# Kernel tuning notes

Hardware: AMD Instinct MI355X
Metric: run time of the kernel (lower is better)

Reference implementation:

```python
import jax, jax.numpy as jnp
import numpy as np

D_MODEL = 2048
N_HEADS = 32
N_KV = 8
HEAD_DIM = D_MODEL // N_HEADS        # 64
N_GROUPS = N_HEADS // N_KV           # 4
ROPE_BASE = 10000.0
SCALE = HEAD_DIM ** -0.5
BATCH, SEQ = 2, 2048


def setup_inputs() -> dict:
    key = jax.random.key(0)
    k1, k2, k3, k4, k5 = jax.random.split(key, 5)
    init = 0.02  # typical transformer init scale
    return {
        "x":  jax.random.normal(k1, (BATCH, SEQ, D_MODEL), jnp.float32),
        "Wq": jax.random.normal(k2, (D_MODEL, D_MODEL), jnp.float32) * init,
        "Wk": jax.random.normal(k3, (N_KV * HEAD_DIM, D_MODEL), jnp.float32) * init,
        "Wv": jax.random.normal(k4, (N_KV * HEAD_DIM, D_MODEL), jnp.float32) * init,
        "Wo": jax.random.normal(k5, (D_MODEL, D_MODEL), jnp.float32) * init,
    }


def _apply_rope(q, k, seq_len):
    # q: (b, n_heads, s, hd), k: (b, n_kv, s, hd). LLaMA-style rotate-half RoPE.
    half = HEAD_DIM // 2
    inv_freq = 1.0 / (ROPE_BASE ** (jnp.arange(0, half, dtype=jnp.float32) / half))
    ang = jnp.arange(seq_len, dtype=jnp.float32)[:, None] * inv_freq[None, :]  # (s, half)
    cos = jnp.concatenate([jnp.cos(ang), jnp.cos(ang)], axis=-1)[None, None]   # (1,1,s,hd)
    sin = jnp.concatenate([jnp.sin(ang), jnp.sin(ang)], axis=-1)[None, None]

    def rot_half(t):
        t1, t2 = jnp.split(t, 2, axis=-1)
        return jnp.concatenate([-t2, t1], axis=-1)

    q = q * cos + rot_half(q) * sin
    k = k * cos + rot_half(k) * sin
    return q, k


def reference(x, Wq, Wk, Wv, Wo):
    b, s, _ = x.shape
    # projections (nn.Linear: y = x @ W.T)
    q = jnp.einsum('bsd,ed->bse', x, Wq).reshape(b, s, N_HEADS, HEAD_DIM).transpose(0, 2, 1, 3)
    k = jnp.einsum('bsd,ed->bse', x, Wk).reshape(b, s, N_KV, HEAD_DIM).transpose(0, 2, 1, 3)
    v = jnp.einsum('bsd,ed->bse', x, Wv).reshape(b, s, N_KV, HEAD_DIM).transpose(0, 2, 1, 3)

    q, k = _apply_rope(q, k, s)

    # GQA: repeat_interleave(k, n_groups) maps q-head h -> kv-head h // n_groups,
    # equivalent to grouping consecutive q heads and broadcasting kv per group.
    qg = q.reshape(b, N_KV, N_GROUPS, s, HEAD_DIM)
    scores = jnp.einsum('bkgqd,bkld->bkgql', qg, k) * SCALE   # (b, n_kv, g, s, s)
    attn = jax.nn.softmax(scores, axis=-1)
    out = jnp.einsum('bkgql,bkld->bkgqd', attn, v)            # (b, n_kv, g, s, hd)

    out = out.reshape(b, N_HEADS, s, HEAD_DIM).transpose(0, 2, 1, 3).reshape(b, s, D_MODEL)
    return jnp.einsum('bsd,ed->bse', out, Wo)
```

## Files before the change

kernel.cpp:

```cpp
#include <hip/hip_runtime.h>
#include <hip/hip_bf16.h>


typedef __attribute__((ext_vector_type(8))) short short8;
typedef __attribute__((ext_vector_type(4))) float f32x4;
typedef __attribute__((ext_vector_type(16))) float f32x16;

#define MFMA16(A, B, C) __builtin_amdgcn_mfma_f32_16x16x32_bf16((A), (B), (C), 0, 0, 0)
#define MFMA32(A, B, C) __builtin_amdgcn_mfma_f32_32x32x16_bf16((A), (B), (C), 0, 0, 0)

__device__ __forceinline__ ushort f2bf(float f) {
  __hip_bfloat16 h = __float2bfloat16(f);
  return __builtin_bit_cast(ushort, h);
}

__device__ __forceinline__ float fexp2(float x) {
#if __has_builtin(__builtin_amdgcn_exp2f)
  return __builtin_amdgcn_exp2f(x);
#else
  float r;
  asm("v_exp_f32 %0, %1" : "=v"(r) : "v"(x));
  return r;
#endif
}

__device__ __forceinline__ void gload_lds16(const void* g, void* l) {
  __builtin_amdgcn_global_load_lds(
      (const __attribute__((address_space(1))) unsigned int*)g,
      (__attribute__((address_space(3))) unsigned int*)l, 16, 0, 0);
}

__global__ __launch_bounds__(256) void prep_kernel(
    const float* __restrict__ x, const float* __restrict__ Wq,
    const float* __restrict__ Wk, const float* __restrict__ Wv,
    const float* __restrict__ Wo, ushort* __restrict__ xbf,
    ushort* __restrict__ wqbf, ushort* __restrict__ wkbf,
    ushort* __restrict__ wvbf, ushort* __restrict__ wobf,
    float* __restrict__ tc, float* __restrict__ ts) {
  const int blk = blockIdx.x;
  if (blk < 9216) {
    const float* src;
    ushort* dst;
    int t;
    if (blk < 4096) {
      src = x; dst = xbf; t = blk * 256 + threadIdx.x;
    } else if (blk < 6144) {
      src = Wq; dst = wqbf; t = (blk - 4096) * 256 + threadIdx.x;
    } else if (blk < 6656) {
      src = Wk; dst = wkbf; t = (blk - 6144) * 256 + threadIdx.x;
    } else if (blk < 7168) {
      src = Wv; dst = wvbf; t = (blk - 6656) * 256 + threadIdx.x;
    } else {
      src = Wo; dst = wobf; t = (blk - 7168) * 256 + threadIdx.x;
    }
    const float4* p = (const float4*)src;
    float4 a = p[t * 2], b = p[t * 2 + 1];
    int4 o;
    o.x = (int)f2bf(a.x) | ((int)f2bf(a.y) << 16);
    o.y = (int)f2bf(a.z) | ((int)f2bf(a.w) << 16);
    o.z = (int)f2bf(b.x) | ((int)f2bf(b.y) << 16);
    o.w = (int)f2bf(b.z) | ((int)f2bf(b.w) << 16);
    ((int4*)dst)[t] = o;
  } else {
    int t = (blk - 9216) * 256 + threadIdx.x;
    int j = t & 31, s = t >> 5;
    float freq = powf(10000.0f, -(float)j * (1.0f / 32.0f));
    float ang = (float)s * freq;
    tc[t] = cosf(ang);
    ts[t] = sinf(ang);
  }
}

__device__ __forceinline__ void gemm_core(const ushort* __restrict__ A,
                                          const ushort* __restrict__ Bt,
                                          int row0, int col0, int K,
                                          f32x4 (&acc)[4][4]) {
  __shared__ __align__(16) ushort As[8192];
  __shared__ __align__(16) ushort Bs[8192];
  const int t = threadIdx.x;
  const int lane = t & 63, wid = t >> 6;
  const int lr = lane & 15, lh = lane >> 4;
  const int wm = wid >> 1, wn = wid & 1;
#pragma unroll
  for (int i = 0; i < 4; ++i)
#pragma unroll
    for (int j = 0; j < 4; ++j) acc[i][j] = (f32x4){0.f, 0.f, 0.f, 0.f};

  const int srow = t >> 3, scg = (t & 7) ^ (srow & 7);
  const ushort* Asrc = A + (size_t)(row0 + srow) * K + scg * 8;
  const ushort* Bsrc = Bt + (size_t)(col0 + srow) * K + scg * 8;
  char* AsB = (char*)As + wid * 1024;
  char* BsB = (char*)Bs + wid * 1024;
  const int s7a = lr & 7;

  for (int k0 = 0; k0 < K; k0 += 64) {
    __syncthreads();
#pragma unroll
    for (int i = 0; i < 4; ++i) {
      gload_lds16(Asrc + (size_t)(32 * i) * K + k0, AsB + i * 4096);
      gload_lds16(Bsrc + (size_t)(32 * i) * K + k0, BsB + i * 4096);
    }
    __syncthreads();

    short8 af[4][2];
#pragma unroll
    for (int fm = 0; fm < 4; ++fm)
#pragma unroll
      for (int kk = 0; kk < 2; ++kk)
        af[fm][kk] = *(const short8*)((const char*)As +
                                      ((wm * 64 + fm * 16 + lr) << 7) +
                                      (((kk * 4 + lh) ^ s7a) << 4));
#pragma unroll
    for (int kk = 0; kk < 2; ++kk)
#pragma unroll
      for (int fn = 0; fn < 4; ++fn) {
        short8 bf_ = *(const short8*)((const char*)Bs +
                                      ((wn * 64 + fn * 16 + lr) << 7) +
                                      (((kk * 4 + lh) ^ s7a) << 4));
#pragma unroll
        for (int fm = 0; fm < 4; ++fm)
          acc[fm][fn] = MFMA16(af[fm][kk], bf_, acc[fm][fn]);
      }
  }
}

__global__ __launch_bounds__(256) void gemm_qkv_kernel(
    const ushort* __restrict__ xbf, const ushort* __restrict__ wq,
    const ushort* __restrict__ wk, const ushort* __restrict__ wv,
    ushort* __restrict__ Qo, ushort* __restrict__ Ko, ushort* __restrict__ Vo,
    const float* __restrict__ tabc, const float* __restrict__ tabs) {
  int bx = blockIdx.x % 24, by = blockIdx.x / 24;
  const ushort* Bt;
  int cb;
  if (bx < 16) {
    Bt = wq; cb = bx;
  } else if (bx < 20) {
    Bt = wk; cb = bx - 16;
  } else {
    Bt = wv; cb = bx - 20;
  }
  f32x4 acc[4][4];
  gemm_core(xbf, Bt, by * 128, cb * 128, 2048, acc);

  const int lane = threadIdx.x & 63, wid = threadIdx.x >> 6;
  const int lr = lane & 15, lh = lane >> 4;
  const int wm = wid >> 1, wn = wid & 1;
  const int srow0 = by * 128 + wm * 64 + lh * 4;

  if (bx >= 20) {
    const int kv = cb * 2 + wn;
#pragma unroll
    for (int fm = 0; fm < 4; ++fm) {
      int srow = srow0 + fm * 16;
      int bb = srow >> 11, s = srow & 2047;
#pragma unroll
      for (int fn = 0; fn < 4; ++fn) {
        int d = fn * 16 + lr;
        ushort4 o;
        o.x = f2bf(acc[fm][fn][0]);
        o.y = f2bf(acc[fm][fn][1]);
        o.z = f2bf(acc[fm][fn][2]);
        o.w = f2bf(acc[fm][fn][3]);
        *(ushort4*)&Vo[((size_t)((bb * 8 + kv) * 64 + d)) * 2048 + s] = o;
      }
    }
  } else {
    ushort* dst;
    int nh, h;
    float scale;
    if (bx < 16) {
      dst = Qo; nh = 32; h = bx * 2 + wn;
      scale = 0.125f * 1.44269504088896340736f;
    } else {
      dst = Ko; nh = 8; h = cb * 2 + wn; scale = 1.0f;
    }
#pragma unroll
    for (int fm = 0; fm < 4; ++fm) {
      int srow = srow0 + fm * 16;
      int bb = srow >> 11, sbase = srow & 2047;
      size_t obase = (size_t)(bb * nh + h) * 2048;
#pragma unroll
      for (int fn = 0; fn < 2; ++fn) {
        int j = fn * 16 + lr;
#pragma unroll
        for (int r = 0; r < 4; ++r) {
          int s = sbase + r;
          float c = tabc[s * 32 + j], sn = tabs[s * 32 + j];
          float x1 = acc[fm][fn][r], x2 = acc[fm][fn + 2][r];
          ushort* po = &dst[(obase + s) * 64 + j];
          po[0] = f2bf((x1 * c - x2 * sn) * scale);
          po[32] = f2bf((x2 * c + x1 * sn) * scale);
        }
      }
    }
  }
}

__global__ __launch_bounds__(256) void gemm_o_kernel(const ushort* __restrict__ A,
                                                     const ushort* __restrict__ Wo,
                                                     float* __restrict__ C) {
  int bx = blockIdx.x & 15, by = blockIdx.x >> 4;
  int row0 = by * 128, col0 = bx * 128;
  f32x4 acc[4][4];
  gemm_core(A, Wo, row0, col0, 2048, acc);
  const int lane = threadIdx.x & 63, wid = threadIdx.x >> 6;
  const int lr = lane & 15, lh = lane >> 4;
  const int wm = wid >> 1, wn = wid & 1;
#pragma unroll
  for (int fm = 0; fm < 4; ++fm) {
    int r0 = row0 + wm * 64 + fm * 16 + lh * 4;
#pragma unroll
    for (int fn = 0; fn < 4; ++fn) {
      int cc = col0 + wn * 64 + fn * 16 + lr;
#pragma unroll
      for (int r = 0; r < 4; ++r) C[(size_t)(r0 + r) * 2048 + cc] = acc[fm][fn][r];
    }
  }
}

__global__ __launch_bounds__(256, 2) void attn_kernel(const ushort* __restrict__ Q,
                                                      const ushort* __restrict__ Kg,
                                                      const ushort* __restrict__ Vt,
                                                      ushort* __restrict__ O) {
  __shared__ __align__(16) char smem_c[32768];
  const int tid = threadIdx.x;
  const int lane = tid & 63;
  const int wid = tid >> 6;
  const int bid = ((blockIdx.x & 7) << 6) | (blockIdx.x >> 3);
  const int qp = bid & 31;
  const int kvh = (bid >> 5) & 7;
  const int b = bid >> 8;
  const int h = kvh * 4 + wid;
  const int q0 = qp * 64;
  const int l31 = lane & 31;
  const int hi = lane >> 5;

  const ushort* Qp = Q + ((size_t)((b * 32 + h) * 2048 + q0)) * 64;
  const ushort* Kp = Kg + ((size_t)((b * 8 + kvh) * 2048)) * 64;
  const ushort* Vp = Vt + ((size_t)((b * 8 + kvh) * 64)) * 2048;

  const int srow = tid >> 3, scg = (tid & 7) ^ (srow & 7);
  const ushort* Kst = Kp + (size_t)srow * 64 + scg * 8;
  const ushort* Vst = Vp + (size_t)srow * 2048 + scg * 8;

#define STAGE(PAR, KV0)                                                         \
  do {                                                                          \
    char* kd_ = smem_c + (PAR) * 8192 + wid * 1024;                             \
    char* vd_ = smem_c + 16384 + (PAR) * 8192 + wid * 1024;                     \
    gload_lds16(Kst + (size_t)(KV0) * 64, kd_);                                 \
    gload_lds16(Kst + (size_t)((KV0) + 32) * 64, kd_ + 4096);                   \
    gload_lds16(Vst + (KV0), vd_);                                              \
    gload_lds16(Vst + 32 * 2048 + (KV0), vd_ + 4096);                           \
  } while (0)

  STAGE(0, 0);

  const short8 qfA0 = *(const short8*)(Qp + (size_t)l31 * 64 + 0 + hi * 8);
  const short8 qfA1 = *(const short8*)(Qp + (size_t)l31 * 64 + 16 + hi * 8);
  const short8 qfA2 = *(const short8*)(Qp + (size_t)l31 * 64 + 32 + hi * 8);
  const short8 qfA3 = *(const short8*)(Qp + (size_t)l31 * 64 + 48 + hi * 8);
  const short8 qfB0 = *(const short8*)(Qp + (size_t)(32 + l31) * 64 + 0 + hi * 8);
  const short8 qfB1 = *(const short8*)(Qp + (size_t)(32 + l31) * 64 + 16 + hi * 8);
  const short8 qfB2 = *(const short8*)(Qp + (size_t)(32 + l31) * 64 + 32 + hi * 8);
  const short8 qfB3 = *(const short8*)(Qp + (size_t)(32 + l31) * 64 + 48 + hi * 8);

  const int s7 = l31 & 7;
  const int ok0 = l31 * 128 + (((0 + hi) ^ s7) << 4);
  const int ok1 = l31 * 128 + (((2 + hi) ^ s7) << 4);
  const int ok2 = l31 * 128 + (((4 + hi) ^ s7) << 4);
  const int ok3 = l31 * 128 + (((6 + hi) ^ s7) << 4);

  f32x16 accA0, accA1, accB0, accB1, kz;
#pragma unroll
  for (int r = 0; r < 16; ++r) {
    accA0[r] = 0.f;
    accA1[r] = 0.f;
    accB0[r] = 0.f;
    accB1[r] = 0.f;
    kz[r] = 0.f;
  }
  float lshA = 0.f, lshB = 0.f;

#define QK2(STA, STB, KOFF)                                  \
  do {                                                       \
    const char* kb_ = smem_c + (KOFF);                       \
    short8 kf_ = *(const short8*)(kb_ + ok0);                \
    __builtin_amdgcn_s_setprio(1);                           \
    STA = MFMA32(kf_, qfA0, kz);                             \
    STB = MFMA32(kf_, qfB0, kz);                             \
    kf_ = *(const short8*)(kb_ + ok1);                       \
    STA = MFMA32(kf_, qfA1, STA);                            \
    STB = MFMA32(kf_, qfB1, STB);                            \
    kf_ = *(const short8*)(kb_ + ok2);                       \
    STA = MFMA32(kf_, qfA2, STA);                            \
    STB = MFMA32(kf_, qfB2, STB);                            \
    kf_ = *(const short8*)(kb_ + ok3);                       \
    STA = MFMA32(kf_, qfA3, STA);                            \
    STB = MFMA32(kf_, qfB3, STB);                            \
    __builtin_amdgcn_s_setprio(0);                           \
  } while (0)

#define SMX(ST, F0, F1, LSH)                                                  \
  do {                                                                        \
    float ps_ = 0.f;                                                          \
    uint pk0_, pk1_, pk2_, pk3_, pk4_, pk5_, pk6_, pk7_;                      \
    _Pragma("unroll") for (int j = 0; j < 8; ++j) {                           \
      float pa_ = fexp2(ST[2 * j]);                                           \
      float pb_ = fexp2(ST[2 * j + 1]);                                       \
      ps_ += pa_ + pb_;                                                       \
      uint w_ = __builtin_amdgcn_perm(__builtin_bit_cast(uint, pb_),          \
                                      __builtin_bit_cast(uint, pa_),          \
                                      0x07060302u);                           \
      switch (j) {                                                            \
        case 0: pk0_ = w_; break;                                             \
        case 1: pk1_ = w_; break;                                             \
        case 2: pk2_ = w_; break;                                             \
        case 3: pk3_ = w_; break;                                             \
        case 4: pk4_ = w_; break;                                             \
        case 5: pk5_ = w_; break;                                             \
        case 6: pk6_ = w_; break;                                             \
        default: pk7_ = w_; break;                                            \
      }                                                                       \
    }                                                                         \
    LSH += ps_;                                                               \
    uint u0_ = hi ? pk0_ : pk2_; u0_ = __shfl_xor(u0_, 32);                   \
    uint u1_ = hi ? pk1_ : pk3_; u1_ = __shfl_xor(u1_, 32);                   \
    uint u2_ = hi ? pk4_ : pk6_; u2_ = __shfl_xor(u2_, 32);                   \
    uint u3_ = hi ? pk5_ : pk7_; u3_ = __shfl_xor(u3_, 32);                   \
    F0.u[0] = hi ? u0_ : pk0_;                                                \
    F0.u[1] = hi ? u1_ : pk1_;                                                \
    F0.u[2] = hi ? pk2_ : u0_;                                                \
    F0.u[3] = hi ? pk3_ : u1_;                                                \
    F1.u[0] = hi ? u2_ : pk4_;                                                \
    F1.u[1] = hi ? u3_ : pk5_;                                                \
    F1.u[2] = hi ? pk6_ : u2_;                                                \
    F1.u[3] = hi ? pk7_ : u3_;                                                \
  } while (0)

#define SMPV2(STA, STB, VOFF, VSX)                                           \
  do {                                                                       \
    union { uint u[4]; short8 s; } fA0_, fA1_, fB0_, fB1_;                   \
    SMX(STA, fA0_, fA1_, lshA);                                              \
    SMX(STB, fB0_, fB1_, lshB);                                              \
    const char* vb_ = smem_c + (VOFF);                                       \
    short8 v0_ = *(const short8*)(vb_ + (ok0 ^ (VSX)));                      \
    short8 v1_ = *(const short8*)(vb_ + (ok1 ^ (VSX)));                      \
    __builtin_amdgcn_s_setprio(1);                                           \
    accA0 = MFMA32(v0_, fA0_.s, accA0);                                      \
    accA0 = MFMA32(v1_, fA1_.s, accA0);                                      \
    accB0 = MFMA32(v0_, fB0_.s, accB0);                                      \
    accB0 = MFMA32(v1_, fB1_.s, accB0);                                      \
    __builtin_amdgcn_s_setprio(0);                                           \
    v0_ = *(const short8*)(vb_ + (ok0 ^ (VSX)) + 4096);                      \
    v1_ = *(const short8*)(vb_ + (ok1 ^ (VSX)) + 4096);                      \
    __builtin_amdgcn_s_setprio(1);                                           \
    accA1 = MFMA32(v0_, fA0_.s, accA1);                                      \
    accA1 = MFMA32(v1_, fA1_.s, accA1);                                      \
    accB1 = MFMA32(v0_, fB0_.s, accB1);                                      \
    accB1 = MFMA32(v1_, fB1_.s, accB1);                                      \
    __builtin_amdgcn_s_setprio(0);                                           \
  } while (0)

  for (int t = 0; t < 32; ++t) {
    asm volatile("s_waitcnt vmcnt(0)" ::: "memory");
    __builtin_amdgcn_s_barrier();
    if (t < 31) STAGE((t + 1) & 1, (t + 1) * 64);
    {
      const int kb = (t & 1) * 8192;
      const int vb = 16384 + (t & 1) * 8192;
      f32x16 stA0_, stB0_, stA1_, stB1_;
      QK2(stA0_, stB0_, kb);
      QK2(stA1_, stB1_, kb + 4096);
      SMPV2(stA0_, stB0_, vb, 0);
      SMPV2(stA1_, stB1_, vb, 64);
    }
  }
#undef STAGE
#undef QK2
#undef SMX
#undef SMPV2

  const float lsA = lshA + __shfl_xor(lshA, 32);
  const float lsB = lshB + __shfl_xor(lshB, 32);
  const float invA = 1.0f / lsA;
  const float invB = 1.0f / lsB;
  ushort* ObA = O + (size_t)(b * 2048 + q0 + l31) * 2048 + h * 64;
  ushort* ObB = O + (size_t)(b * 2048 + q0 + 32 + l31) * 2048 + h * 64;
#pragma unroll
  for (int rg = 0; rg < 4; ++rg) {
    ushort4 o0, o1;
    o0.x = f2bf(accA0[rg * 4 + 0] * invA);
    o0.y = f2bf(accA0[rg * 4 + 1] * invA);
    o0.z = f2bf(accA0[rg * 4 + 2] * invA);
    o0.w = f2bf(accA0[rg * 4 + 3] * invA);
    o1.x = f2bf(accA1[rg * 4 + 0] * invA);
    o1.y = f2bf(accA1[rg * 4 + 1] * invA);
    o1.z = f2bf(accA1[rg * 4 + 2] * invA);
    o1.w = f2bf(accA1[rg * 4 + 3] * invA);
    *(ushort4*)(ObA + rg * 8 + hi * 4) = o0;
    *(ushort4*)(ObA + 32 + rg * 8 + hi * 4) = o1;
    o0.x = f2bf(accB0[rg * 4 + 0] * invB);
    o0.y = f2bf(accB0[rg * 4 + 1] * invB);
    o0.z = f2bf(accB0[rg * 4 + 2] * invB);
    o0.w = f2bf(accB0[rg * 4 + 3] * invB);
    o1.x = f2bf(accB1[rg * 4 + 0] * invB);
    o1.y = f2bf(accB1[rg * 4 + 1] * invB);
    o1.z = f2bf(accB1[rg * 4 + 2] * invB);
    o1.w = f2bf(accB1[rg * 4 + 3] * invB);
    *(ushort4*)(ObB + rg * 8 + hi * 4) = o0;
    *(ushort4*)(ObB + 32 + rg * 8 + hi * 4) = o1;
  }
}

extern "C" void kernel_launch(void* const* d_in, const int* in_sizes, int n_in,
                              void* d_out, int out_size, void* d_ws, size_t ws_size,
                              hipStream_t stream) {
  (void)in_sizes; (void)n_in; (void)out_size; (void)ws_size;
  const float* x = (const float*)d_in[0];
  const float* Wq = (const float*)d_in[1];
  const float* Wk = (const float*)d_in[2];
  const float* Wv = (const float*)d_in[3];
  const float* Wo = (const float*)d_in[4];
  float* out = (float*)d_out;

  char* ws = (char*)d_ws;
  size_t off = 0;
  auto take = [&](size_t bytes) {
    void* p = ws + off;
    off += (bytes + 255) & ~(size_t)255;
    return p;
  };
  ushort* xbf = (ushort*)take(16777216);
  ushort* wqbf = (ushort*)take(8388608);
  ushort* wkbf = (ushort*)take(2097152);
  ushort* wvbf = (ushort*)take(2097152);
  ushort* wobf = (ushort*)take(8388608);
  ushort* Qbf = (ushort*)take(16777216);
  ushort* Kbf = (ushort*)take(4194304);
  ushort* Vtb = (ushort*)take(4194304);
  ushort* attnout = (ushort*)take(16777216);
  float* tabc = (float*)take(262144);
  float* tabs = (float*)take(262144);

  prep_kernel<<<9472, 256, 0, stream>>>(x, Wq, Wk, Wv, Wo, xbf, wqbf, wkbf,
                                        wvbf, wobf, tabc, tabs);
  gemm_qkv_kernel<<<768, 256, 0, stream>>>(xbf, wqbf, wkbf, wvbf, Qbf, Kbf,
                                           Vtb, tabc, tabs);
  attn_kernel<<<512, 256, 0, stream>>>(Qbf, Kbf, Vtb, attnout);
  gemm_o_kernel<<<512, 256, 0, stream>>>(attnout, wobf, out);
}
```

Baseline: 209.1 us.

## Double-buffer LDS tiles in output projection GEMM

Adds a double-buffered GEMM core that prefetches the next K-tile into a second LDS buffer via direct global-to-LDS loads while MFMAs run on the current one. The output projection kernel now uses it, with launch bounds requesting two blocks per CU. The aim is to hide global load latency behind compute. The cost is doubled LDS use (64KB per block) and possible register pressure, which may limit occupancy.

New measurement: 205.8 us (median of 3 runs). About the same (-1.6%).

```diff
diff --git a/kernel.cpp b/kernel.cpp
--- a/kernel.cpp
+++ b/kernel.cpp
@@ -124,6 +124,72 @@
   }
 }
 
+__device__ __forceinline__ void gemm_core_db(const ushort* __restrict__ A,
+                                             const ushort* __restrict__ Bt,
+                                             int row0, int col0, int K,
+                                             f32x4 (&acc)[4][4]) {
+  __shared__ __align__(16) ushort As[16384];
+  __shared__ __align__(16) ushort Bs[16384];
+  const int t = threadIdx.x;
+  const int lane = t & 63, wid = t >> 6;
+  const int lr = lane & 15, lh = lane >> 4;
+  const int wm = wid >> 1, wn = wid & 1;
+#pragma unroll
+  for (int i = 0; i < 4; ++i)
+#pragma unroll
+    for (int j = 0; j < 4; ++j) acc[i][j] = (f32x4){0.f, 0.f, 0.f, 0.f};
+
+  const int srow = t >> 3, scg = (t & 7) ^ (srow & 7);
+  const ushort* Asrc = A + (size_t)(row0 + srow) * K + scg * 8;
+  const ushort* Bsrc = Bt + (size_t)(col0 + srow) * K + scg * 8;
+  const int s7a = lr & 7;
+
+#define GSTAGE(PAR, KOFF)                                                    \
+  do {                                                                       \
+    char* a_ = (char*)As + (PAR) * 16384 + wid * 1024;                       \
+    char* b_ = (char*)Bs + (PAR) * 16384 + wid * 1024;                       \
+    _Pragma("unroll") for (int i_ = 0; i_ < 4; ++i_) {                       \
+      gload_lds16(Asrc + (size_t)(32 * i_) * K + (KOFF), a_ + i_ * 4096);    \
+      gload_lds16(Bsrc + (size_t)(32 * i_) * K + (KOFF), b_ + i_ * 4096);    \
+    }                                                                        \
+  } while (0)
+
+  GSTAGE(0, 0);
+  GSTAGE(1, 64);
+  const int nstep = K >> 6;
+  for (int it = 0; it < nstep; ++it) {
+    if (it + 1 < nstep)
+      asm volatile("s_waitcnt vmcnt(8)" ::: "memory");
+    else
+      asm volatile("s_waitcnt vmcnt(0)" ::: "memory");
+    __builtin_amdgcn_s_barrier();
+    {
+      const char* ab_ = (const char*)As + (it & 1) * 16384;
+      const char* bb_ = (const char*)Bs + (it & 1) * 16384;
+      short8 af[4][2];
+#pragma unroll
+      for (int fm = 0; fm < 4; ++fm)
+#pragma unroll
+        for (int kk = 0; kk < 2; ++kk)
+          af[fm][kk] = *(const short8*)(ab_ + ((wm * 64 + fm * 16 + lr) << 7) +
+                                        (((kk * 4 + lh) ^ s7a) << 4));
+#pragma unroll
+      for (int kk = 0; kk < 2; ++kk)
+#pragma unroll
+        for (int fn = 0; fn < 4; ++fn) {
+          short8 bf_ = *(const short8*)(bb_ + ((wn * 64 + fn * 16 + lr) << 7) +
+                                        (((kk * 4 + lh) ^ s7a) << 4));
+#pragma unroll
+          for (int fm = 0; fm < 4; ++fm)
+            acc[fm][fn] = MFMA16(af[fm][kk], bf_, acc[fm][fn]);
+        }
+    }
+    __builtin_amdgcn_s_barrier();
+    if (it + 2 < nstep) GSTAGE(it & 1, (it + 2) * 64);
+  }
+#undef GSTAGE
+}
+
 __global__ __launch_bounds__(256) void gemm_qkv_kernel(
     const ushort* __restrict__ xbf, const ushort* __restrict__ wq,
     const ushort* __restrict__ wk, const ushort* __restrict__ wv,
@@ -196,13 +262,13 @@
   }
 }
 
-__global__ __launch_bounds__(256) void gemm_o_kernel(const ushort* __restrict__ A,
-                                                     const ushort* __restrict__ Wo,
-                                                     float* __restrict__ C) {
+__global__ __launch_bounds__(256, 2) void gemm_o_kernel(const ushort* __restrict__ A,
+                                                        const ushort* __restrict__ Wo,
+                                                        float* __restrict__ C) {
   int bx = blockIdx.x & 15, by = blockIdx.x >> 4;
   int row0 = by * 128, col0 = bx * 128;
   f32x4 acc[4][4];
-  gemm_core(A, Wo, row0, col0, 2048, acc);
+  gemm_core_db(A, Wo, row0, col0, 2048, acc);
   const int lane = threadIdx.x & 63, wid = threadIdx.x >> 6;
   const int lr = lane & 15, lh = lane >> 4;
   const int wm = wid >> 1, wn = wid & 1;
```
